# Performance work log

Measured on AMD Instinct MI355X. Metric: run time of the kernel, lower is better.

The kernel has to match this reference:

```python
import jax, jax.numpy as jnp
import numpy as np

B, T_ENC, H, L, V = 32, 1024, 1024, 511, 512
SOS = 0


def setup_inputs() -> dict:
    key = jax.random.key(0)
    ks = jax.random.split(key, 16)
    s = 0.02
    inp = {
        "encoder_outputs": jax.random.normal(ks[0], (B, T_ENC, H), jnp.float32),
        "encoder_output_lengths": jnp.clip(
            jax.random.randint(ks[1], (B,), 0, T_ENC), 1, T_ENC
        ).astype(jnp.int64 if jax.config.jax_enable_x64 else jnp.int32),
        "input_labels": jax.random.randint(ks[2], (B, L), 0, V),
        # parameters
        "emb": jax.random.normal(ks[3], (V, H), jnp.float32) * s,
        "lin_in": jax.random.normal(ks[4], (H, H), jnp.float32) * s,      # attention linear_in (no bias)
        "lin_out": jax.random.normal(ks[5], (H, 2 * H), jnp.float32) * s,  # attention linear_out (no bias)
        "gru_w_ih0": jax.random.normal(ks[6], (3 * H, H), jnp.float32) * s,
        "gru_w_hh0": jax.random.normal(ks[7], (3 * H, H), jnp.float32) * s,
        "gru_b_ih0": jax.random.normal(ks[8], (3 * H,), jnp.float32) * s,
        "gru_b_hh0": jax.random.normal(ks[9], (3 * H,), jnp.float32) * s,
        "gru_w_ih1": jax.random.normal(ks[10], (3 * H, H), jnp.float32) * s,
        "gru_w_hh1": jax.random.normal(ks[11], (3 * H, H), jnp.float32) * s,
        "gru_b_ih1": jax.random.normal(ks[12], (3 * H,), jnp.float32) * s,
        "gru_b_hh1": jax.random.normal(ks[13], (3 * H,), jnp.float32) * s,
        "fc_w": jax.random.normal(ks[14], (V, H), jnp.float32) * s,
        "fc_b": jax.random.normal(ks[15], (V,), jnp.float32) * s,
    }
    return inp


def _gru_layer(x_proj, w_hh, b_hh):
    """x_proj: [B, T, 3H] precomputed input projection (incl. b_ih). Torch gate order r,z,n."""
    h0 = jnp.zeros((x_proj.shape[0], w_hh.shape[1]), x_proj.dtype)

    def step(h, xp):
        gh = h @ w_hh.T + b_hh
        xr, xz, xn = jnp.split(xp, 3, axis=-1)
        hr, hz, hn = jnp.split(gh, 3, axis=-1)
        r = jax.nn.sigmoid(xr + hr)
        z = jax.nn.sigmoid(xz + hz)
        n = jnp.tanh(xn + r * hn)
        h_new = (1.0 - z) * n + z * h
        return h_new, h_new

    _, ys = jax.lax.scan(step, h0, x_proj.transpose(1, 0, 2))
    return ys.transpose(1, 0, 2)  # [B, T, H]


def reference(encoder_outputs, encoder_output_lengths, input_labels, emb,
              lin_in, lin_out, gru_w_ih0, gru_w_hh0, gru_b_ih0, gru_b_hh0,
              gru_w_ih1, gru_w_hh1, gru_b_ih1, gru_b_hh1, fc_w, fc_b):
    Bsz = encoder_outputs.shape[0]
    # prepend SOS token (teacher forcing path)
    labels = jnp.concatenate(
        [jnp.full((Bsz, 1), SOS, dtype=input_labels.dtype), input_labels], axis=1
    )  # [B, L+1]
    x = emb[labels]  # [B, L+1, H] (dropout p=0 -> identity)

    # Attention (type='general')
    q = jnp.einsum("bqd,ed->bqe", x, lin_in)  # linear_in(query)
    scores = jnp.einsum("bqd,bkd->bqk", q, encoder_outputs)  # [B, L+1, T]
    t = encoder_outputs.shape[1]
    mask = jnp.arange(t)[None, :] >= encoder_output_lengths[:, None]  # [B, T]
    scores = jnp.where(mask[:, None, :], -jnp.inf, scores)
    w = jax.nn.softmax(scores, axis=-1)
    mix = jnp.einsum("bqk,bkd->bqd", w, encoder_outputs)
    combined = jnp.concatenate([mix, q], axis=-1)  # [B, L+1, 2H]
    attn_out = jnp.tanh(jnp.einsum("bqc,dc->bqd", combined, lin_out))

    # 2-layer GRU (rnn2)
    xp0 = jnp.einsum("btd,gd->btg", attn_out, gru_w_ih0) + gru_b_ih0
    y0 = _gru_layer(xp0, gru_w_hh0, gru_b_hh0)
    xp1 = jnp.einsum("btd,gd->btg", y0, gru_w_ih1) + gru_b_ih1
    y1 = _gru_layer(xp1, gru_w_hh1, gru_b_hh1)

    logits = jnp.einsum("btd,vd->btv", y1, fc_w) + fc_b
    return jax.nn.log_softmax(logits, axis=-1)  # [B, L+1, V]
```

## Files before the change

### kernel.cpp

```cpp
#include <hip/hip_runtime.h>

typedef unsigned short u16;
typedef unsigned int u32;
typedef short bs8 __attribute__((ext_vector_type(8)));
typedef float f4_t __attribute__((ext_vector_type(4)));

#define NB   32
#define TSEQ 512
#define TENC 1024
#define HD   1024
#define VOC  512
#define FS   32
#define POLL_CAP (1 << 22)

#define AS1 __attribute__((address_space(1)))
#define AS3 __attribute__((address_space(3)))

__device__ __forceinline__ float b2f(u16 u) {
  union { u32 i; float f; } x; x.i = ((u32)u) << 16; return x.f;
}
__device__ __forceinline__ u16 f2b(float f) {
  union { float ff; u32 i; } x; x.ff = f;
  u32 r = x.i + 0x7fff + ((x.i >> 16) & 1);
  return (u16)(r >> 16);
}
__device__ __forceinline__ float inF(const void* p, size_t i, int bf) {
  return bf ? b2f(((const u16*)p)[i]) : ((const float*)p)[i];
}
__device__ __forceinline__ void inF4(const void* p, size_t i, int bf, float* o) {
  if (bf) {
    ushort4 u = *reinterpret_cast<const ushort4*>((const u16*)p + i);
    o[0] = b2f(u.x); o[1] = b2f(u.y); o[2] = b2f(u.z); o[3] = b2f(u.w);
  } else {
    float4 v = *reinterpret_cast<const float4*>((const float*)p + i);
    o[0] = v.x; o[1] = v.y; o[2] = v.z; o[3] = v.w;
  }
}
__device__ __forceinline__ void outF(void* p, size_t i, float v, int bf) {
  if (bf) ((u16*)p)[i] = f2b(v);
  else ((float*)p)[i] = v;
}
__device__ __forceinline__ void gld16(const void* g, void* l) {
  __builtin_amdgcn_global_load_lds((const AS1 u32*)g, (AS3 u32*)l, 16, 0, 0);
}
__device__ __forceinline__ u32 aLoad(u32* p) {
  return __hip_atomic_load(p, __ATOMIC_RELAXED, __HIP_MEMORY_SCOPE_AGENT);
}
__device__ __forceinline__ void aStore(u32* p, u32 v) {
  __hip_atomic_store(p, v, __ATOMIC_RELAXED, __HIP_MEMORY_SCOPE_AGENT);
}
__device__ __forceinline__ uint4 ldUC(const char* p) {
  uint4 r;
  asm volatile("global_load_dwordx4 %0, %1, off sc0 sc1" : "=v"(r) : "v"(p));
  return r;
}
__device__ __forceinline__ void stUCshort(char* p, u32 v) {
  asm volatile("global_store_short %0, %1, off sc0 sc1" :: "v"(p), "v"(v) : "memory");
}
__device__ __forceinline__ void waitVM0() {
  asm volatile("s_waitcnt vmcnt(0)" ::: "memory");
}

__global__ void k_detect(const u32* __restrict__ w, int* __restrict__ flag) {
  __shared__ int cnt;
  if (threadIdx.x == 0) cnt = 0;
  __syncthreads();
  int c = 0;
  for (int i = threadIdx.x; i < 1024; i += 256) {
    u32 e = (w[i] >> 7) & 0xFF;
    if (e >= 100 && e <= 126) c++;
  }
  atomicAdd(&cnt, c);
  __syncthreads();
  if (threadIdx.x == 0) flag[0] = (cnt >= 512) ? 1 : 0;
}

__global__ __launch_bounds__(256) void k_f2bf(
    const void* __restrict__ in, u16* __restrict__ out, const int* __restrict__ flagp) {
  const int bf = flagp[0];
  size_t i = ((size_t)blockIdx.x * 256 + threadIdx.x) * 4;
  float v[4]; inF4(in, i, bf, v);
  ushort4 o; o.x = f2b(v[0]); o.y = f2b(v[1]); o.z = f2b(v[2]); o.w = f2b(v[3]);
  *reinterpret_cast<ushort4*>(&out[i]) = o;
}

__global__ __launch_bounds__(256) void k_embed(
    const int* __restrict__ labels, const void* __restrict__ emb,
    u16* __restrict__ x, const int* __restrict__ flagp) {
  const int bf = flagp[0];
  const int m = blockIdx.x;
  const int b = m >> 9, t = m & 511;
  const int lab = (t == 0) ? 0 : labels[b * 511 + t - 1];
  const size_t src = (size_t)lab * HD;
  const size_t dst = (size_t)m * HD;
  const int k = threadIdx.x * 4;
  float v[4]; inF4(emb, src + k, bf, v);
  ushort4 o; o.x = f2b(v[0]); o.y = f2b(v[1]); o.z = f2b(v[2]); o.w = f2b(v[3]);
  *reinterpret_cast<ushort4*>(&x[dst + k]) = o;
}

__global__ __launch_bounds__(256) void k_transpose(
    const void* __restrict__ enc, u16* __restrict__ encT, const int* __restrict__ flagp) {
  const int bf = flagp[0];
  __shared__ float tile[32][33];
  const int b = blockIdx.z, t0 = blockIdx.x * 32, h0 = blockIdx.y * 32;
  const int i = threadIdx.x >> 5, j = threadIdx.x & 31;
  const size_t base = (size_t)b * (TENC * HD);
#pragma unroll
  for (int rr = 0; rr < 4; rr++) {
    int r = i + rr * 8;
    tile[r][j] = inF(enc, base + (size_t)(t0 + r) * HD + h0 + j, bf);
  }
  __syncthreads();
#pragma unroll
  for (int rr = 0; rr < 4; rr++) {
    int r = i + rr * 8;
    encT[base + (size_t)(h0 + r) * TENC + t0 + j] = f2b(tile[j][r]);
  }
}

__global__ __launch_bounds__(256) void k_mfma_gemm(
    const u16* __restrict__ A, const u16* __restrict__ Bm, int K, int lda, int ldb,
    long strideA, long strideB, long strideC,
    void* __restrict__ C, int ldc, int cmode, int act,
    const void* __restrict__ bias, const int* __restrict__ flagp) {
  const int bf = flagp[0];
  __shared__ u16 lsA[8192];
  __shared__ u16 lsB[8192];
  const int tid = threadIdx.x;
  const int l = tid & 63, w = tid >> 6;
  const int wr = w >> 1, wc = w & 1;
  const long m0 = (long)blockIdx.x * 128;
  const long n0 = (long)blockIdx.y * 128;
  const long bz = blockIdx.z;
  const u16* Ab = A + bz * strideA;
  const u16* Bb = Bm + bz * strideB;

  f4_t acc[4][4] = {};
  const int srow = w * 8 + (l >> 3);
  const int schx = (l & 7) * 16;

  for (int kt = 0; kt < K; kt += 64) {
#pragma unroll
    for (int i = 0; i < 4; i++) {
      const int row = i * 32 + srow;
      const char* ga = (const char*)(Ab + (m0 + row) * (long)lda + kt)
                       + (schx ^ ((row & 7) << 4));
      gld16(ga, (char*)lsA + i * 4096 + w * 1024);
    }
#pragma unroll
    for (int i = 0; i < 4; i++) {
      const int row = i * 32 + srow;
      const char* gb = (const char*)(Bb + (n0 + row) * (long)ldb + kt)
                       + (schx ^ ((row & 7) << 4));
      gld16(gb, (char*)lsB + i * 4096 + w * 1024);
    }
    __syncthreads();
#pragma unroll
    for (int h = 0; h < 2; h++) {
      bs8 af[4], bfr[4];
#pragma unroll
      for (int i = 0; i < 4; i++) {
        const int row = wr * 64 + i * 16 + (l & 15);
        const int byt = row * 128 + (((h * 64) + ((l >> 4) * 16)) ^ ((row & 7) << 4));
        af[i] = *(const bs8*)((const char*)lsA + byt);
      }
#pragma unroll
      for (int j = 0; j < 4; j++) {
        const int row = wc * 64 + j * 16 + (l & 15);
        const int byt = row * 128 + (((h * 64) + ((l >> 4) * 16)) ^ ((row & 7) << 4));
        bfr[j] = *(const bs8*)((const char*)lsB + byt);
      }
#pragma unroll
      for (int i = 0; i < 4; i++)
#pragma unroll
        for (int j = 0; j < 4; j++)
          acc[i][j] = __builtin_amdgcn_mfma_f32_16x16x32_bf16(af[i], bfr[j], acc[i][j], 0, 0, 0);
    }
    __syncthreads();
  }

  float bv[4] = {0.f, 0.f, 0.f, 0.f};
  if (bias) {
#pragma unroll
    for (int j = 0; j < 4; j++)
      bv[j] = inF(bias, (size_t)(n0 + wc * 64 + j * 16 + (l & 15)), bf);
  }
#pragma unroll
  for (int i = 0; i < 4; i++) {
#pragma unroll
    for (int j = 0; j < 4; j++) {
      const long rowb = m0 + wr * 64 + i * 16 + ((l >> 4) * 4);
      const long col = n0 + wc * 64 + j * 16 + (l & 15);
#pragma unroll
      for (int r = 0; r < 4; r++) {
        float v = acc[i][j][r] + bv[j];
        if (act == 1) v = tanhf(v);
        const long row = rowb + r;
        if (cmode == 0) {
          ((u16*)C)[bz * strideC + row * (long)ldc + col] = f2b(v);
        } else if (cmode == 1) {
          ((float*)C)[bz * strideC + row * (long)ldc + col] = v;
        } else {
          ((u16*)C)[((long)(row & 511) * 32 + (row >> 9)) * (long)ldc + col] = f2b(v);
        }
      }
    }
  }
}

__global__ __launch_bounds__(256) void k_softmax(
    u16* __restrict__ S, const int* __restrict__ lens) {
  const int m = blockIdx.x;
  const int b = m >> 9;
  const int len = lens[b];
  const int tid = threadIdx.x;
  const size_t base = (size_t)m * TENC;
  float v[4];
  float mx = -1e30f;
#pragma unroll
  for (int i = 0; i < 4; i++) {
    int j = tid + i * 256;
    float s = b2f(S[base + j]);
    v[i] = (j < len) ? s : -1e30f;
    mx = fmaxf(mx, v[i]);
  }
  __shared__ float red[8];
  for (int o = 32; o; o >>= 1) mx = fmaxf(mx, __shfl_xor(mx, o, 64));
  if ((tid & 63) == 0) red[tid >> 6] = mx;
  __syncthreads();
  mx = fmaxf(fmaxf(red[0], red[1]), fmaxf(red[2], red[3]));
  float e[4]; float sum = 0.f;
#pragma unroll
  for (int i = 0; i < 4; i++) {
    e[i] = (v[i] > -1e29f) ? expf(v[i] - mx) : 0.f;
    sum += e[i];
  }
  for (int o = 32; o; o >>= 1) sum += __shfl_xor(sum, o, 64);
  __shared__ float red2[8];
  if ((tid & 63) == 0) red2[tid >> 6] = sum;
  __syncthreads();
  sum = red2[0] + red2[1] + red2[2] + red2[3];
  const float inv = 1.f / sum;
#pragma unroll
  for (int i = 0; i < 4; i++) S[base + tid + i * 256] = f2b(e[i] * inv);
}

__global__ __launch_bounds__(256) void k_packw(
    const void* __restrict__ Wih, const void* __restrict__ Whh,
    u16* __restrict__ out, int fused, const int* __restrict__ flagp) {
  const int bf = flagp[0];
  const long idx = (long)blockIdx.x * 256 + threadIdx.x;
  const int l = (int)(idx & 63);
  int ks, c16, blk;
  if (fused) { ks = (int)((idx >> 6) & 63); c16 = (int)((idx >> 12) & 1); blk = (int)(idx >> 13); }
  else       { ks = (int)((idx >> 6) & 31); c16 = (int)((idx >> 11) & 1); blk = (int)(idx >> 12); }
  const int v = blk * 32 + c16 * 16 + (l & 15);
  const int f = v >> 2, slot = v & 3;
  const int k = ks * 32 + ((l >> 4) << 3);
  const void* W = Whh; long row = 0; bool zero = false; int kk = k;
  if (!fused) {
    if (slot == 0) row = f;
    else if (slot == 1) row = 1024 + f;
    else if (slot == 2) row = 2048 + f;
    else zero = true;
  } else {
    const bool xp = (k < 1024); kk = k & 1023;
    W = xp ? Wih : Whh;
    if (slot == 0) row = f;
    else if (slot == 1) row = 1024 + f;
    else if (slot == 2) { row = 2048 + f; zero = !xp; }
    else { row = 2048 + f; zero = xp; }
  }
  u16 o[8];
#pragma unroll
  for (int e = 0; e < 8; e++)
    o[e] = zero ? (u16)0 : f2b(inF(W, (size_t)row * 1024 + kk + e, bf));
  ushort4* dst = (ushort4*)(out + idx * 8);
  dst[0] = make_ushort4(o[0], o[1], o[2], o[3]);
  dst[1] = make_ushort4(o[4], o[5], o[6], o[7]);
}

__device__ __forceinline__ void stage64(const char* src, char* dst, int tid) {
#pragma unroll
  for (int bh = 0; bh < 2; bh++) {
    uint4 v[8];
#pragma unroll
    for (int i = 0; i < 8; i++)
      v[i] = ldUC(src + (bh * 8 + i) * 4096 + tid * 16);
    waitVM0();
#pragma unroll
    for (int i = 0; i < 8; i++)
      *(uint4*)(dst + (bh * 8 + i) * 4096 + tid * 16) = v[i];
  }
}
__device__ __forceinline__ void waitpair(u32* flags, int aL0, int aL1, int tid) {
  if (tid < 64) {
    int guard = 0;
    while (1) {
      const int v0 = (int)aLoad(flags + (size_t)tid * FS);
      const int v1 = (int)aLoad(flags + (size_t)(tid + 64) * FS);
      const int v2 = (int)aLoad(flags + (size_t)(tid + 128) * FS);
      const int v3 = (int)aLoad(flags + (size_t)(tid + 192) * FS);
      const bool ok = (v0 >= aL0) && (v1 >= aL0) && (v2 >= aL1) && (v3 >= aL1);
      if (__all(ok)) break;
      if (++guard > POLL_CAP) break;
      __builtin_amdgcn_s_sleep(1);
    }
  }
  __syncthreads();
}

__global__ void __launch_bounds__(256, 1) k_gru_p(
    const u16* __restrict__ xp0, const u16* __restrict__ wpk0, const u16* __restrict__ wpk1,
    const void* __restrict__ bhh0, const void* __restrict__ bih1, const void* __restrict__ bhh1,
    u16* __restrict__ y1, char* h0buf, char* h1buf, u32* flags,
    const int* __restrict__ flagp) {
  extern __shared__ char smem[];
  float* red = (float*)(smem + 131072);
  const int bf = flagp[0];
  const int tid = threadIdx.x, l = tid & 63, w = tid >> 6;
  const int nh = w & 1, kh = w >> 1;
  const int g = blockIdx.x;
  const bool isL0 = (g < 128);
  const int gg = isL0 ? g : g - 128;
  const int fl = (l & 15) >> 2;
  const int F = gg * 8 + nh * 4 + fl;
  const int bl0 = (l & 48) | (fl << 2);

  float hprev[2][4] = {{0.f, 0.f, 0.f, 0.f}, {0.f, 0.f, 0.f, 0.f}};

  if (isL0) {
    {
      const char* wsrc = (const char*)(wpk0 + (size_t)gg * 32768);
#pragma unroll
      for (int i = 0; i < 16; i++) {
        const int off = i * 4096 + w * 1024;
        gld16(wsrc + off + l * 16, smem + off);
      }
    }
    __syncthreads();
    const char* Wl = smem;
    char* img = smem + 65536;
    const float br = inF(bhh0, (size_t)F, bf);
    const float bz = inF(bhh0, (size_t)(1024 + F), bf);
    const float bn = inF(bhh0, (size_t)(2048 + F), bf);
    for (int t = 0; t < TSEQ; t++) {
      waitpair(flags, t, t - 1, tid);
      stage64(h0buf + (t & 1) * 65536, img, tid);
      __syncthreads();
      f4_t S[2] = {};
#pragma unroll 4
      for (int ksl = 0; ksl < 16; ksl++) {
        const int ks = kh * 16 + ksl;
        const bs8 bb = *(const bs8*)(Wl + (((size_t)(nh * 32 + ks) * 64 + l) << 4));
#pragma unroll
        for (int mt = 0; mt < 2; mt++) {
          const int row = mt * 16 + (l & 15);
          const int byt = row * 2048 + ((ks * 64 + ((l >> 4) << 4)) ^ ((row & 7) << 4));
          const bs8 aa = *(const bs8*)(img + byt);
          S[mt] = __builtin_amdgcn_mfma_f32_16x16x32_bf16(aa, bb, S[mt], 0, 0, 0);
        }
      }
      if (kh == 1) {
#pragma unroll
        for (int mt = 0; mt < 2; mt++)
          *(f4_t*)&red[((nh * 2 + mt) * 64 + l) * 4] = S[mt];
      }
      __syncthreads();
      if (kh == 0) {
#pragma unroll
        for (int mt = 0; mt < 2; mt++)
          S[mt] += *(const f4_t*)&red[((nh * 2 + mt) * 64 + l) * 4];
        char* hw = h0buf + ((t + 1) & 1) * 65536;
#pragma unroll
        for (int mt = 0; mt < 2; mt++) {
#pragma unroll
          for (int r = 0; r < 4; r++) {
            const int b = mt * 16 + ((l >> 4) << 2) + r;
            const float hr = __shfl(S[mt][r], bl0);
            const float hz = __shfl(S[mt][r], bl0 + 1);
            const float hn = __shfl(S[mt][r], bl0 + 2);
            const long xb = (long)t * 98304 + (long)b * 3072 + F;
            const float xr = b2f(xp0[xb]);
            const float xz = b2f(xp0[xb + 1024]);
            const float xn = b2f(xp0[xb + 2048]);
            const float rr = 1.f / (1.f + expf(-(xr + hr + br)));
            const float zz = 1.f / (1.f + expf(-(xz + hz + bz)));
            const float nn = tanhf(xn + rr * (hn + bn));
            const float hv = (1.f - zz) * nn + zz * hprev[mt][r];
            hprev[mt][r] = hv;
            if ((l & 3) == 0) {
              const int swb = b * 2048 + ((2 * F) ^ ((b & 7) << 4));
              stUCshort(hw + swb, (u32)f2b(hv));
            }
          }
        }
      }
      waitVM0();
      __syncthreads();
      if (tid == 0) aStore(flags + (size_t)g * FS, (u32)(t + 1));
    }
  } else {
    const char* W = (const char*)(wpk1 + (size_t)gg * 65536);
    for (int s = 0; s < TSEQ; s++) {
      const float br = inF(bih1, (size_t)F, bf) + inF(bhh1, (size_t)F, bf);
      const float bz = inF(bih1, (size_t)(1024 + F), bf) + inF(bhh1, (size_t)(1024 + F), bf);
      const float bxn = inF(bih1, (size_t)(2048 + F), bf);
      const float bhn = inF(bhh1, (size_t)(2048 + F), bf);
      waitpair(flags, s + 1, s, tid);
      stage64(h0buf + ((s + 1) & 1) * 65536, smem, tid);
      stage64(h1buf + (s & 1) * 65536, smem + 65536, tid);
      __syncthreads();
      f4_t S[2] = {};
#pragma unroll 4
      for (int ksl = 0; ksl < 32; ksl++) {
        const int ks = kh * 32 + ksl;
        const bs8 bb = *(const bs8*)(W + (((size_t)(nh * 64 + ks) * 64 + l) << 4));
        const int base = (ks >= 32) ? 65536 : 0;
        const int ks5 = ks & 31;
#pragma unroll
        for (int mt = 0; mt < 2; mt++) {
          const int row = mt * 16 + (l & 15);
          const int byt = base + row * 2048 + ((ks5 * 64 + ((l >> 4) << 4)) ^ ((row & 7) << 4));
          const bs8 aa = *(const bs8*)(smem + byt);
          S[mt] = __builtin_amdgcn_mfma_f32_16x16x32_bf16(aa, bb, S[mt], 0, 0, 0);
        }
      }
      if (kh == 1) {
#pragma unroll
        for (int mt = 0; mt < 2; mt++)
          *(f4_t*)&red[((nh * 2 + mt) * 64 + l) * 4] = S[mt];
      }
      __syncthreads();
      if (kh == 0) {
#pragma unroll
        for (int mt = 0; mt < 2; mt++)
          S[mt] += *(const f4_t*)&red[((nh * 2 + mt) * 64 + l) * 4];
        char* hw = h1buf + ((s + 1) & 1) * 65536;
#pragma unroll
        for (int mt = 0; mt < 2; mt++) {
#pragma unroll
          for (int r = 0; r < 4; r++) {
            const int b = mt * 16 + ((l >> 4) << 2) + r;
            const float rs = __shfl(S[mt][r], bl0);
            const float zs = __shfl(S[mt][r], bl0 + 1);
            const float xnp = __shfl(S[mt][r], bl0 + 2);
            const float hnp = __shfl(S[mt][r], bl0 + 3);
            const float rr = 1.f / (1.f + expf(-(rs + br)));
            const float zz = 1.f / (1.f + expf(-(zs + bz)));
            const float nn = tanhf((xnp + bxn) + rr * (hnp + bhn));
            const float hv = (1.f - zz) * nn + zz * hprev[mt][r];
            hprev[mt][r] = hv;
            if ((l & 3) == 0) {
              const int swb = b * 2048 + ((2 * F) ^ ((b & 7) << 4));
              stUCshort(hw + swb, (u32)f2b(hv));
              y1[((long)b * 512 + s) * 1024 + F] = f2b(hv);
            }
          }
        }
      }
      waitVM0();
      __syncthreads();
      if (tid == 0) aStore(flags + (size_t)g * FS, (u32)(s + 1));
    }
  }
}

__global__ __launch_bounds__(256) void k_logsoftmax(
    const float* __restrict__ L, void* __restrict__ out, const int* __restrict__ flagp) {
  const int bf = flagp[0];
  const int m = blockIdx.x;
  const int tid = threadIdx.x;
  const size_t base = (size_t)m * VOC;
  float v0 = L[base + tid], v1 = L[base + tid + 256];
  float mx = fmaxf(v0, v1);
  __shared__ float red[8];
  for (int o = 32; o; o >>= 1) mx = fmaxf(mx, __shfl_xor(mx, o, 64));
  if ((tid & 63) == 0) red[tid >> 6] = mx;
  __syncthreads();
  mx = fmaxf(fmaxf(red[0], red[1]), fmaxf(red[2], red[3]));
  float s = expf(v0 - mx) + expf(v1 - mx);
  for (int o = 32; o; o >>= 1) s += __shfl_xor(s, o, 64);
  __shared__ float red2[8];
  if ((tid & 63) == 0) red2[tid >> 6] = s;
  __syncthreads();
  s = red2[0] + red2[1] + red2[2] + red2[3];
  const float lse = mx + logf(s);
  outF(out, base + tid, v0 - lse, bf);
  outF(out, base + tid + 256, v1 - lse, bf);
}

extern "C" void kernel_launch(void* const* d_in, const int* in_sizes, int n_in,
                              void* d_out, int out_size, void* d_ws, size_t ws_size,
                              hipStream_t stream) {
  const void* enc = d_in[0];
  const int* lens = (const int*)d_in[1];
  const int* labels = (const int*)d_in[2];
  const void* emb = d_in[3];
  const void* lin_in = d_in[4];
  const void* lin_out = d_in[5];
  const void* w_ih0 = d_in[6];
  const void* w_hh0 = d_in[7];
  const void* b_ih0 = d_in[8];
  const void* b_hh0 = d_in[9];
  const void* w_ih1 = d_in[10];
  const void* w_hh1 = d_in[11];
  const void* b_ih1 = d_in[12];
  const void* b_hh1 = d_in[13];
  const void* fc_w = d_in[14];
  const void* fc_b = d_in[15];

  char* ws = (char*)d_ws;
  const size_t SZ = (size_t)NB * TSEQ * HD * 2;
  int* flag = (int*)ws;
  u16* R0 = (u16*)(ws + 256);
  u16* R1 = (u16*)(ws + 256 + SZ);
  u16* R2 = (u16*)(ws + 256 + 2 * SZ);
  char* R4 = ws + 256 + 4 * SZ;

  char* R2u = (char*)R2 + SZ;
  u16* wpk0 = (u16*)R2u;
  u16* wpk1 = (u16*)(R2u + 8388608);
  char* hreg = R2u + 25165824;
  u32* flagsbuf = (u32*)hreg;
  char* h0buf = hreg + 32768;
  char* h1buf = hreg + 32768 + 131072;
  const size_t hreg_bytes = 32768 + 262144;

  u16* scores = (u16*)R4;
  u16* wli = (u16*)(R4 + 35651584);
  u16* wlo = (u16*)(R4 + 37748736);
  u16* xp0 = (u16*)R4;
  u16* wfc = (u16*)R4;
  float* logits = (float*)(R4 + 1048576);

  k_detect<<<1, 256, 0, stream>>>((const u32*)emb, flag);
  k_embed<<<NB * TSEQ, 256, 0, stream>>>(labels, emb, R0, flag);
  k_f2bf<<<32768, 256, 0, stream>>>(enc, R1, flag);
  k_f2bf<<<1024, 256, 0, stream>>>(lin_in, wli, flag);
  k_f2bf<<<2048, 256, 0, stream>>>(lin_out, wlo, flag);

  k_mfma_gemm<<<dim3(128, 8, 1), 256, 0, stream>>>(
      R0, wli, HD, HD, HD, 0, 0, 0, (void*)(R2 + 1024), 2 * HD, 0, 0, nullptr, flag);
  k_transpose<<<dim3(32, 32, NB), 256, 0, stream>>>(enc, R0, flag);
  k_mfma_gemm<<<dim3(4, 8, NB), 256, 0, stream>>>(
      R2 + 1024, R1, HD, 2 * HD, HD,
      (long)TSEQ * 2 * HD, (long)TENC * HD, (long)TSEQ * TENC,
      (void*)scores, TENC, 0, 0, nullptr, flag);
  k_softmax<<<NB * TSEQ, 256, 0, stream>>>(scores, lens);
  k_mfma_gemm<<<dim3(4, 8, NB), 256, 0, stream>>>(
      scores, R0, TENC, TENC, TENC,
      (long)TSEQ * TENC, (long)HD * TENC, (long)TSEQ * 2 * HD,
      (void*)R2, 2 * HD, 0, 0, nullptr, flag);
  k_mfma_gemm<<<dim3(128, 8, 1), 256, 0, stream>>>(
      R2, wlo, 2 * HD, 2 * HD, 2 * HD, 0, 0, 0,
      (void*)R0, HD, 0, 1, nullptr, flag);

  k_packw<<<2048, 256, 0, stream>>>(nullptr, w_hh0, wpk0, 0, flag);
  k_packw<<<4096, 256, 0, stream>>>(w_ih1, w_hh1, wpk1, 1, flag);
  k_f2bf<<<3072, 256, 0, stream>>>(w_ih0, R1, flag);
  k_mfma_gemm<<<dim3(128, 24, 1), 256, 0, stream>>>(
      R0, R1, HD, HD, HD, 0, 0, 0, (void*)xp0, 3 * HD, 2, 0, b_ih0, flag);

  hipMemsetAsync(hreg, 0, hreg_bytes, stream);
  hipFuncSetAttribute((const void*)k_gru_p,
                      hipFuncAttributeMaxDynamicSharedMemorySize, 139264);
  u16* y1p = R2;
  void* args[] = {&xp0, &wpk0, &wpk1,
                  (void*)&b_hh0, (void*)&b_ih1, (void*)&b_hh1,
                  &y1p, &h0buf, &h1buf, &flagsbuf, &flag};
  hipLaunchCooperativeKernel((const void*)k_gru_p, dim3(256), dim3(256),
                             args, 139264, stream);

  k_f2bf<<<512, 256, 0, stream>>>(fc_w, wfc, flag);
  k_mfma_gemm<<<dim3(128, 4, 1), 256, 0, stream>>>(
      R2, wfc, HD, HD, HD, 0, 0, 0, (void*)logits, VOC, 1, 0, fc_b, flag);
  k_logsoftmax<<<NB * TSEQ, 256, 0, stream>>>(logits, d_out, flag);
}
```

Measured before the change: 5.827 ms.

## Replace per-block flag polling with two shared atomic step counters in GRU kernel

The cross-block barrier in the persistent GRU kernel previously had a full wavefront poll 256 per-block flags, padded to separate cache lines. Each layer now has one global counter that every block atomically increments after each timestep, and a single thread polls the two counters until they reach 128*t. This cuts polling traffic and the wave-wide vote, but all 128 blocks of a layer now contend on one atomic address. The sleep interval and the poll cap are also raised.

```diff
diff --git a/kernel.cpp b/kernel.cpp
--- a/kernel.cpp
+++ b/kernel.cpp
@@ -10,8 +10,7 @@
 #define TENC 1024
 #define HD   1024
 #define VOC  512
-#define FS   32
-#define POLL_CAP (1 << 22)
+#define POLL_CAP (1 << 24)
 
 #define AS1 __attribute__((address_space(1)))
 #define AS3 __attribute__((address_space(3)))
@@ -45,9 +44,6 @@
 }
 __device__ __forceinline__ u32 aLoad(u32* p) {
   return __hip_atomic_load(p, __ATOMIC_RELAXED, __HIP_MEMORY_SCOPE_AGENT);
-}
-__device__ __forceinline__ void aStore(u32* p, u32 v) {
-  __hip_atomic_store(p, v, __ATOMIC_RELAXED, __HIP_MEMORY_SCOPE_AGENT);
 }
 __device__ __forceinline__ uint4 ldUC(const char* p) {
   uint4 r;
@@ -294,18 +290,15 @@
       *(uint4*)(dst + (bh * 8 + i) * 4096 + tid * 16) = v[i];
   }
 }
-__device__ __forceinline__ void waitpair(u32* flags, int aL0, int aL1, int tid) {
-  if (tid < 64) {
-    int guard = 0;
+__device__ __forceinline__ void waitcnts(u32* c0, u32* c1, long t0, long t1, int tid) {
+  if (tid == 0) {
+    long guard = 0;
     while (1) {
-      const int v0 = (int)aLoad(flags + (size_t)tid * FS);
-      const int v1 = (int)aLoad(flags + (size_t)(tid + 64) * FS);
-      const int v2 = (int)aLoad(flags + (size_t)(tid + 128) * FS);
-      const int v3 = (int)aLoad(flags + (size_t)(tid + 192) * FS);
-      const bool ok = (v0 >= aL0) && (v1 >= aL0) && (v2 >= aL1) && (v3 >= aL1);
-      if (__all(ok)) break;
+      const long v0 = (long)aLoad(c0);
+      const long v1 = (long)aLoad(c1);
+      if (v0 >= t0 && v1 >= t1) break;
       if (++guard > POLL_CAP) break;
-      __builtin_amdgcn_s_sleep(1);
+      __builtin_amdgcn_s_sleep(2);
     }
   }
   __syncthreads();
@@ -314,7 +307,7 @@
 __global__ void __launch_bounds__(256, 1) k_gru_p(
     const u16* __restrict__ xp0, const u16* __restrict__ wpk0, const u16* __restrict__ wpk1,
     const void* __restrict__ bhh0, const void* __restrict__ bih1, const void* __restrict__ bhh1,
-    u16* __restrict__ y1, char* h0buf, char* h1buf, u32* flags,
+    u16* __restrict__ y1, char* h0buf, char* h1buf, u32* cnts,
     const int* __restrict__ flagp) {
   extern __shared__ char smem[];
   float* red = (float*)(smem + 131072);
@@ -327,6 +320,8 @@
   const int fl = (l & 15) >> 2;
   const int F = gg * 8 + nh * 4 + fl;
   const int bl0 = (l & 48) | (fl << 2);
+  u32* cnt0 = cnts;
+  u32* cnt1 = cnts + 32;
 
   float hprev[2][4] = {{0.f, 0.f, 0.f, 0.f}, {0.f, 0.f, 0.f, 0.f}};
 
@@ -346,7 +341,7 @@
     const float bz = inF(bhh0, (size_t)(1024 + F), bf);
     const float bn = inF(bhh0, (size_t)(2048 + F), bf);
     for (int t = 0; t < TSEQ; t++) {
-      waitpair(flags, t, t - 1, tid);
+      waitcnts(cnt0, cnt1, 128L * t, 128L * (t - 1), tid);
       stage64(h0buf + (t & 1) * 65536, img, tid);
       __syncthreads();
       f4_t S[2] = {};
@@ -399,7 +394,7 @@
       }
       waitVM0();
       __syncthreads();
-      if (tid == 0) aStore(flags + (size_t)g * FS, (u32)(t + 1));
+      if (tid == 0) atomicAdd(cnt0, 1u);
     }
   } else {
     const char* W = (const char*)(wpk1 + (size_t)gg * 65536);
@@ -408,7 +403,7 @@
       const float bz = inF(bih1, (size_t)(1024 + F), bf) + inF(bhh1, (size_t)(1024 + F), bf);
       const float bxn = inF(bih1, (size_t)(2048 + F), bf);
       const float bhn = inF(bhh1, (size_t)(2048 + F), bf);
-      waitpair(flags, s + 1, s, tid);
+      waitcnts(cnt0, cnt1, 128L * (s + 1), 128L * s, tid);
       stage64(h0buf + ((s + 1) & 1) * 65536, smem, tid);
       stage64(h1buf + (s & 1) * 65536, smem + 65536, tid);
       __syncthreads();
@@ -462,7 +457,7 @@
       }
       waitVM0();
       __syncthreads();
-      if (tid == 0) aStore(flags + (size_t)g * FS, (u32)(s + 1));
+      if (tid == 0) atomicAdd(cnt1, 1u);
     }
   }
 }
@@ -523,7 +518,7 @@
   u16* wpk0 = (u16*)R2u;
   u16* wpk1 = (u16*)(R2u + 8388608);
   char* hreg = R2u + 25165824;
-  u32* flagsbuf = (u32*)hreg;
+  u32* cnts = (u32*)hreg;
   char* h0buf = hreg + 32768;
   char* h1buf = hreg + 32768 + 131072;
   const size_t hreg_bytes = 32768 + 262144;
@@ -569,7 +564,7 @@
   u16* y1p = R2;
   void* args[] = {&xp0, &wpk0, &wpk1,
                   (void*)&b_hh0, (void*)&b_ih1, (void*)&b_hh1,
-                  &y1p, &h0buf, &h1buf, &flagsbuf, &flag};
+                  &y1p, &h0buf, &h1buf, &cnts, &flag};
   hipLaunchCooperativeKernel((const void*)k_gru_p, dim3(256), dim3(256),
                              args, 139264, stream);
 
```

Measured after the change: 8.666 ms. 1.49x slower.
